# Performance work log

Measured on AMD Instinct MI355X. Metric: run time of the kernel, lower is better.

Reference implementation:

```python
import jax, jax.numpy as jnp
import numpy as np

N = 131072
L = 300  # lan_vec_len

def _boxes(k):
    k1, k2, k3, k4 = jax.random.split(k, 4)
    x1 = jax.random.uniform(k1, (N,)) * 500.0
    y1 = jax.random.uniform(k2, (N,)) * 500.0
    w = 1.0 + jax.random.uniform(k3, (N,)) * 200.0
    h = 1.0 + jax.random.uniform(k4, (N,)) * 200.0
    return x1, y1, x1 + w, y1 + h

def setup_inputs() -> dict:
    key = jax.random.key(0)
    ks = jax.random.split(key, 10)
    sbj_vec = jax.random.normal(ks[0], (N, L), jnp.float32)
    obj_vec = jax.random.normal(ks[1], (N, L), jnp.float32)
    sx1, sy1, sx2, sy2 = _boxes(ks[2])
    ox1, oy1, ox2, oy2 = _boxes(ks[3])
    label = jax.random.randint(ks[4], (N,), 0, 2).astype(jnp.float32)
    misc = jax.random.uniform(ks[5], (N,))
    # rlts columns: [0:4 misc, 4 label, 5:9 sbj box, 9 misc, 10:14 obj box, 14 misc]
    rlts = jnp.stack([misc, misc, misc, misc, label,
                      sx1, sy1, sx2, sy2, misc,
                      ox1, oy1, ox2, oy2, misc], axis=1)
    spa_w = jax.random.normal(ks[6], (8, 1), jnp.float32) * 0.1
    spa_b = jnp.zeros((1,), jnp.float32)
    lan_w1 = jax.random.normal(ks[7], (2 * L, L), jnp.float32) * 0.05
    lan_b1 = jnp.zeros((L,), jnp.float32)
    lan_w2 = jax.random.normal(ks[8], (L, 1), jnp.float32) * 0.05
    lan_b2 = jnp.zeros((1,), jnp.float32)
    return {"sbj_vec": sbj_vec, "obj_vec": obj_vec, "rlts": rlts,
            "spa_w": spa_w, "spa_b": spa_b,
            "lan_w1": lan_w1, "lan_b1": lan_b1,
            "lan_w2": lan_w2, "lan_b2": lan_b2}

def _ext_box_feat(rlts):
    sb = rlts[:, 5:9]
    ob = rlts[:, 10:14]
    sw = sb[:, 2] - sb[:, 0]
    sh = sb[:, 3] - sb[:, 1]
    ow = ob[:, 2] - ob[:, 0]
    oh = ob[:, 3] - ob[:, 1]
    sbj = jnp.stack([(sb[:, 0] - ob[:, 0]) / sw,
                     (sb[:, 1] - ob[:, 1]) / sh,
                     jnp.log(sw / ow), jnp.log(sh / oh)], axis=1)
    obj = jnp.stack([(ob[:, 0] - sb[:, 0]) / ow,
                     (ob[:, 1] - sb[:, 1]) / oh,
                     jnp.log(ow / sw), jnp.log(oh / sh)], axis=1)
    return sbj, obj

def reference(sbj_vec, obj_vec, rlts, spa_w, spa_b, lan_w1, lan_b1, lan_w2, lan_b2):
    sbj_box, obj_box = _ext_box_feat(rlts)
    lan_feat = jnp.concatenate([sbj_vec, obj_vec], axis=1)        # [N, 2L]
    box_feat = jnp.concatenate([sbj_box, obj_box], axis=1)        # [N, 8]
    # lan_stream: ReLU -> (Dropout: identity in eval) -> Linear -> ReLU -> Linear
    h = jax.nn.relu(lan_feat)
    h = jax.nn.relu(h @ lan_w1 + lan_b1)
    lan_scores = h @ lan_w2 + lan_b2                              # [N, 1]
    box_scores = box_feat @ spa_w + spa_b                         # [N, 1]
    scores = jax.nn.sigmoid(lan_scores + box_scores)              # [N, 1]
    ys = (rlts[:, 4] > 0).astype(scores.dtype)                    # [N]
    s = scores[:, 0]
    # binary cross entropy (mean), clamped like torch's BCE
    log_s = jnp.clip(jnp.log(jnp.clip(s, 1e-12, 1.0)), -100.0)
    log_1s = jnp.clip(jnp.log(jnp.clip(1.0 - s, 1e-12, 1.0)), -100.0)
    loss = -jnp.mean(ys * log_s + (1.0 - ys) * log_1s)
    # faithful replication of loss_test's (buggy) counting logic, vectorized
    neg = ys == 0
    pos = ~neg
    N_pos = jnp.sum(pos.astype(jnp.float32))
    N_neg = jnp.sum(neg.astype(jnp.float32))
    N_pos_right = jnp.sum((neg & (s >= 0.5)).astype(jnp.float32))
    N_neg_right = jnp.sum((pos & (s < 0.5)).astype(jnp.float32))
    recall_pos = N_pos_right / N_pos
    recall_neg = N_neg_right / N_neg
    recall_all = (N_pos_right + N_neg_right) / (N_pos + N_neg)
    return scores, loss, recall_pos, recall_neg, recall_all
```

## Files before the change

### kernel.cpp

```cpp
#include <hip/hip_runtime.h>

constexpr int NROWS  = 131072;
constexpr int LDIM   = 300;
constexpr int KDIM   = 600;
constexpr int NPAD   = 320;
constexpr int KGRP   = 76;
constexpr int MTILE  = 128;
constexpr int NBLKS  = NROWS / MTILE;
constexpr int KSTEPS = 19;
constexpr int WT_ELEMS = KGRP * NPAD * 8;
constexpr size_t PART_OFF = 393216;

typedef __bf16 bf16x8 __attribute__((ext_vector_type(8)));
typedef float  f32x16 __attribute__((ext_vector_type(16)));
typedef const unsigned int __attribute__((address_space(1))) gu32;
typedef unsigned int __attribute__((address_space(3))) lu32;

__device__ __forceinline__ unsigned short f2bf(float f) {
    unsigned u = __float_as_uint(f);
    u += 0x7fffu + ((u >> 16) & 1u);
    return (unsigned short)(u >> 16);
}

__global__ void prep_w1(const float* __restrict__ w1, unsigned short* __restrict__ wt) {
    int idx = blockIdx.x * 256 + threadIdx.x;
    if (idx >= WT_ELEMS) return;
    int j    = idx & 7;
    int rest = idx >> 3;
    int n    = rest % NPAD;
    int kg   = rest / NPAD;
    int k    = kg * 8 + j;
    float v = 0.f;
    if (k < KDIM && n < LDIM) v = w1[k * LDIM + n];
    wt[idx] = f2bf(v);
}

__launch_bounds__(256, 2)
__global__ void main_kernel(const float* __restrict__ sbj, const float* __restrict__ obj,
                            const float* __restrict__ rlts,
                            const float* __restrict__ spa_w, const float* __restrict__ spa_b,
                            const float* __restrict__ b1, const float* __restrict__ w2,
                            const float* __restrict__ b2,
                            const unsigned short* __restrict__ wt,
                            float* __restrict__ out_scores, float* __restrict__ part) {
    __shared__ __attribute__((aligned(16))) short A_lds[4 * 128 * 8];
    __shared__ __attribute__((aligned(16))) short B_lds[4 * 320 * 8];
    __shared__ float lanpart[2][128];
    __shared__ float redbuf[4][8];

    const int tid  = threadIdx.x;
    const int lane = tid & 63;
    const int wv   = tid >> 6;
    const int wm   = wv >> 1;
    const int wn   = wv & 1;
    const int l31  = lane & 31;
    const int l5   = lane >> 5;

    const int  blk  = blockIdx.x;
    const long row0 = (long)blk * MTILE;

    const int a_quad = tid & 7;
    const int a_rowb = tid >> 3;

    f32x16 acc[2][5];
    #pragma unroll
    for (int mt = 0; mt < 2; ++mt)
        #pragma unroll
        for (int nt = 0; nt < 5; ++nt)
            acc[mt][nt] = (f32x16)(0.f);

    for (int kt = 0; kt < KSTEPS; ++kt) {
        {
            const unsigned short* src = wt + (size_t)kt * (4 * 320 * 8) + wv * 2560 + lane * 8;
            short* dst = &B_lds[wv * 2560 + lane * 8];
            #pragma unroll
            for (int it = 0; it < 5; ++it) {
                __builtin_amdgcn_global_load_lds((gu32*)(src + it * 512),
                                                 (lu32*)(dst + it * 512), 16, 0, 0);
            }
        }
        {
            const int kglob0 = kt * 32 + a_quad * 4;
            #pragma unroll
            for (int i = 0; i < 4; ++i) {
                const int  row  = a_rowb + i * 32;
                const long grow = row0 + row;
                float4 v;
                if (kglob0 < LDIM) {
                    v = *(const float4*)(sbj + grow * LDIM + kglob0);
                } else if (kglob0 < KDIM) {
                    v = *(const float4*)(obj + grow * LDIM + (kglob0 - LDIM));
                } else {
                    v = make_float4(0.f, 0.f, 0.f, 0.f);
                }
                unsigned h0 = f2bf(fmaxf(v.x, 0.f));
                unsigned h1 = f2bf(fmaxf(v.y, 0.f));
                unsigned h2 = f2bf(fmaxf(v.z, 0.f));
                unsigned h3 = f2bf(fmaxf(v.w, 0.f));
                uint2 pk = make_uint2(h0 | (h1 << 16), h2 | (h3 << 16));
                *(uint2*)&A_lds[((a_quad >> 1) * 128 + row) * 8 + (a_quad & 1) * 4] = pk;
            }
        }
        __syncthreads();
        #pragma unroll
        for (int ki = 0; ki < 2; ++ki) {
            const int half = ki * 2 + l5;
            bf16x8 af[2];
            #pragma unroll
            for (int mt = 0; mt < 2; ++mt) {
                const int row = wm * 64 + mt * 32 + l31;
                af[mt] = *(const bf16x8*)&A_lds[(half * 128 + row) * 8];
            }
            #pragma unroll
            for (int nt = 0; nt < 5; ++nt) {
                const int n = wn * 160 + nt * 32 + l31;
                bf16x8 bfr = *(const bf16x8*)&B_lds[(half * 320 + n) * 8];
                #pragma unroll
                for (int mt = 0; mt < 2; ++mt)
                    acc[mt][nt] = __builtin_amdgcn_mfma_f32_32x32x16_bf16(af[mt], bfr, acc[mt][nt], 0, 0, 0);
            }
        }
        __syncthreads();
    }

    float part_r[2][16];
    #pragma unroll
    for (int mt = 0; mt < 2; ++mt)
        #pragma unroll
        for (int r = 0; r < 16; ++r) part_r[mt][r] = 0.f;

    #pragma unroll
    for (int nt = 0; nt < 5; ++nt) {
        const int n = wn * 160 + nt * 32 + l31;
        if (n < LDIM) {
            const float b1n = b1[n];
            const float w2n = w2[n];
            #pragma unroll
            for (int mt = 0; mt < 2; ++mt)
                #pragma unroll
                for (int r = 0; r < 16; ++r) {
                    float h = fmaxf(acc[mt][nt][r] + b1n, 0.f);
                    part_r[mt][r] = fmaf(h, w2n, part_r[mt][r]);
                }
        }
    }
    #pragma unroll
    for (int off = 1; off < 32; off <<= 1)
        #pragma unroll
        for (int mt = 0; mt < 2; ++mt)
            #pragma unroll
            for (int r = 0; r < 16; ++r)
                part_r[mt][r] += __shfl_xor(part_r[mt][r], off, 64);

    if (l31 == 0) {
        #pragma unroll
        for (int mt = 0; mt < 2; ++mt)
            #pragma unroll
            for (int r = 0; r < 16; ++r) {
                const int rl = wm * 64 + mt * 32 + (r & 3) + 8 * (r >> 2) + 4 * l5;
                lanpart[wn][rl] = part_r[mt][r];
            }
    }
    __syncthreads();

    float s_loss = 0.f, s_cp = 0.f, s_cn = 0.f, s_pr = 0.f, s_nr = 0.f;
    if (tid < 128) {
        const long g   = row0 + tid;
        const float lan = lanpart[0][tid] + lanpart[1][tid] + b2[0];
        const float* rr = rlts + g * 15;
        const float label = rr[4];
        const float sx1 = rr[5],  sy1 = rr[6],  sx2 = rr[7],  sy2 = rr[8];
        const float ox1 = rr[10], oy1 = rr[11], ox2 = rr[12], oy2 = rr[13];
        const float sw = sx2 - sx1, sh = sy2 - sy1, ow = ox2 - ox1, oh = oy2 - oy1;
        float bs = spa_w[0] * ((sx1 - ox1) / sw)
                 + spa_w[1] * ((sy1 - oy1) / sh)
                 + spa_w[2] * logf(sw / ow)
                 + spa_w[3] * logf(sh / oh)
                 + spa_w[4] * ((ox1 - sx1) / ow)
                 + spa_w[5] * ((oy1 - sy1) / oh)
                 + spa_w[6] * logf(ow / sw)
                 + spa_w[7] * logf(oh / sh)
                 + spa_b[0];
        const float z = lan + bs;
        const float s = 1.f / (1.f + expf(-z));
        out_scores[g] = s;
        const float ls = fmaxf(logf(fminf(fmaxf(s, 1e-12f), 1.f)), -100.f);
        const float l1 = fmaxf(logf(fminf(fmaxf(1.f - s, 1e-12f), 1.f)), -100.f);
        const bool ys = label > 0.f;
        s_loss = ys ? ls : l1;
        s_cp   = ys ? 1.f : 0.f;
        s_cn   = ys ? 0.f : 1.f;
        s_pr   = (!ys && s >= 0.5f) ? 1.f : 0.f;
        s_nr   = (ys && s < 0.5f)  ? 1.f : 0.f;
    }
    #pragma unroll
    for (int off = 1; off < 64; off <<= 1) {
        s_loss += __shfl_xor(s_loss, off, 64);
        s_cp   += __shfl_xor(s_cp, off, 64);
        s_cn   += __shfl_xor(s_cn, off, 64);
        s_pr   += __shfl_xor(s_pr, off, 64);
        s_nr   += __shfl_xor(s_nr, off, 64);
    }
    if (lane == 0) {
        redbuf[wv][0] = s_loss; redbuf[wv][1] = s_cp; redbuf[wv][2] = s_cn;
        redbuf[wv][3] = s_pr;   redbuf[wv][4] = s_nr;
    }
    __syncthreads();
    if (tid == 0) {
        float t0 = 0.f, t1 = 0.f, t2 = 0.f, t3 = 0.f, t4 = 0.f;
        for (int w = 0; w < 4; ++w) {
            t0 += redbuf[w][0]; t1 += redbuf[w][1]; t2 += redbuf[w][2];
            t3 += redbuf[w][3]; t4 += redbuf[w][4];
        }
        part[blk * 8 + 0] = t0; part[blk * 8 + 1] = t1; part[blk * 8 + 2] = t2;
        part[blk * 8 + 3] = t3; part[blk * 8 + 4] = t4;
    }
}

__global__ void final_reduce(const float* __restrict__ part, float* __restrict__ out) {
    __shared__ float red[4][8];
    const int tid = threadIdx.x;
    const int lane = tid & 63, wv = tid >> 6;
    float a0 = 0.f, a1 = 0.f, a2 = 0.f, a3 = 0.f, a4 = 0.f;
    for (int b = tid; b < NBLKS; b += 256) {
        a0 += part[b * 8 + 0]; a1 += part[b * 8 + 1]; a2 += part[b * 8 + 2];
        a3 += part[b * 8 + 3]; a4 += part[b * 8 + 4];
    }
    #pragma unroll
    for (int off = 1; off < 64; off <<= 1) {
        a0 += __shfl_xor(a0, off, 64); a1 += __shfl_xor(a1, off, 64);
        a2 += __shfl_xor(a2, off, 64); a3 += __shfl_xor(a3, off, 64);
        a4 += __shfl_xor(a4, off, 64);
    }
    if (lane == 0) { red[wv][0] = a0; red[wv][1] = a1; red[wv][2] = a2; red[wv][3] = a3; red[wv][4] = a4; }
    __syncthreads();
    if (tid == 0) {
        float t0 = 0.f, t1 = 0.f, t2 = 0.f, t3 = 0.f, t4 = 0.f;
        for (int w = 0; w < 4; ++w) {
            t0 += red[w][0]; t1 += red[w][1]; t2 += red[w][2]; t3 += red[w][3]; t4 += red[w][4];
        }
        out[NROWS + 0] = -t0 / (float)NROWS;
        out[NROWS + 1] = t3 / t1;
        out[NROWS + 2] = t4 / t2;
        out[NROWS + 3] = (t3 + t4) / (t1 + t2);
    }
}

extern "C" void kernel_launch(void* const* d_in, const int* in_sizes, int n_in,
                              void* d_out, int out_size, void* d_ws, size_t ws_size,
                              hipStream_t stream) {
    const float* sbj   = (const float*)d_in[0];
    const float* obj   = (const float*)d_in[1];
    const float* rlts  = (const float*)d_in[2];
    const float* spa_w = (const float*)d_in[3];
    const float* spa_b = (const float*)d_in[4];
    const float* w1    = (const float*)d_in[5];
    const float* b1    = (const float*)d_in[6];
    const float* w2    = (const float*)d_in[7];
    const float* b2    = (const float*)d_in[8];
    float* out = (float*)d_out;

    unsigned short* wt = (unsigned short*)d_ws;
    float* part = (float*)((char*)d_ws + PART_OFF);

    prep_w1<<<(WT_ELEMS + 255) / 256, 256, 0, stream>>>(w1, wt);
    main_kernel<<<NBLKS, 256, 0, stream>>>(sbj, obj, rlts, spa_w, spa_b, b1, w2, b2, wt, out, part);
    final_reduce<<<1, 256, 0, stream>>>(part, out);
}
```

Baseline: 404.7 us.

## Shrink row tile, read W1 fragments from global, double-buffer A in LDS

Halves the row tile to 64 rows per block and switches from 32x32 to 16x16x32 MFMA, with each wave covering 80 output columns across all 64 rows. The B (W1) operand is no longer staged through LDS via global_load_lds; each wave reads its bf16 fragments straight from global/L2. A is double-buffered in padded LDS, and the next k-step's global loads are issued before the MFMAs, so only one barrier is needed per step. Occupancy is raised to 3 blocks per CU. This trades more L2 traffic for W1 and twice as many blocks for less LDS use and better latency hiding.

```diff
diff --git a/kernel.cpp b/kernel.cpp
--- a/kernel.cpp
+++ b/kernel.cpp
@@ -5,16 +5,15 @@
 constexpr int KDIM   = 600;
 constexpr int NPAD   = 320;
 constexpr int KGRP   = 76;
-constexpr int MTILE  = 128;
+constexpr int MTILE  = 64;
 constexpr int NBLKS  = NROWS / MTILE;
 constexpr int KSTEPS = 19;
 constexpr int WT_ELEMS = KGRP * NPAD * 8;
 constexpr size_t PART_OFF = 393216;
+constexpr int ASTRIDE = 40;
 
 typedef __bf16 bf16x8 __attribute__((ext_vector_type(8)));
-typedef float  f32x16 __attribute__((ext_vector_type(16)));
-typedef const unsigned int __attribute__((address_space(1))) gu32;
-typedef unsigned int __attribute__((address_space(3))) lu32;
+typedef float  f32x4  __attribute__((ext_vector_type(4)));
 
 __device__ __forceinline__ unsigned short f2bf(float f) {
     unsigned u = __float_as_uint(f);
@@ -35,7 +34,7 @@
     wt[idx] = f2bf(v);
 }
 
-__launch_bounds__(256, 2)
+__launch_bounds__(256, 3)
 __global__ void main_kernel(const float* __restrict__ sbj, const float* __restrict__ obj,
                             const float* __restrict__ rlts,
                             const float* __restrict__ spa_w, const float* __restrict__ spa_b,
@@ -43,130 +42,125 @@
                             const float* __restrict__ b2,
                             const unsigned short* __restrict__ wt,
                             float* __restrict__ out_scores, float* __restrict__ part) {
-    __shared__ __attribute__((aligned(16))) short A_lds[4 * 128 * 8];
-    __shared__ __attribute__((aligned(16))) short B_lds[4 * 320 * 8];
-    __shared__ float lanpart[2][128];
+    __shared__ __attribute__((aligned(16))) short A_lds[2][MTILE * ASTRIDE];
+    __shared__ float lanpart[4][MTILE];
     __shared__ float redbuf[4][8];
 
     const int tid  = threadIdx.x;
     const int lane = tid & 63;
     const int wv   = tid >> 6;
-    const int wm   = wv >> 1;
-    const int wn   = wv & 1;
-    const int l31  = lane & 31;
-    const int l5   = lane >> 5;
+    const int l4   = lane & 15;
+    const int q4   = lane >> 4;
+    const int nbase = wv * 80;
 
     const int  blk  = blockIdx.x;
     const long row0 = (long)blk * MTILE;
 
     const int a_quad = tid & 7;
-    const int a_rowb = tid >> 3;
-
-    f32x16 acc[2][5];
-    #pragma unroll
-    for (int mt = 0; mt < 2; ++mt)
-        #pragma unroll
-        for (int nt = 0; nt < 5; ++nt)
-            acc[mt][nt] = (f32x16)(0.f);
+    const int a_row  = tid >> 3;
+
+    f32x4 acc[4][5];
+    #pragma unroll
+    for (int rt = 0; rt < 4; ++rt)
+        #pragma unroll
+        for (int ct = 0; ct < 5; ++ct)
+            acc[rt][ct] = (f32x4)(0.f);
+
+    float4 pre[2];
+
+    auto load_A = [&](int kt) {
+        const int k0 = kt * 32 + a_quad * 4;
+        #pragma unroll
+        for (int i = 0; i < 2; ++i) {
+            const long grow = row0 + a_row + i * 32;
+            if (k0 < LDIM)       pre[i] = *(const float4*)(sbj + grow * LDIM + k0);
+            else if (k0 < KDIM)  pre[i] = *(const float4*)(obj + grow * LDIM + (k0 - LDIM));
+            else                 pre[i] = make_float4(0.f, 0.f, 0.f, 0.f);
+        }
+    };
+    auto store_A = [&](int buf) {
+        #pragma unroll
+        for (int i = 0; i < 2; ++i) {
+            const int row = a_row + i * 32;
+            unsigned h0 = f2bf(fmaxf(pre[i].x, 0.f));
+            unsigned h1 = f2bf(fmaxf(pre[i].y, 0.f));
+            unsigned h2 = f2bf(fmaxf(pre[i].z, 0.f));
+            unsigned h3 = f2bf(fmaxf(pre[i].w, 0.f));
+            uint2 pk = make_uint2(h0 | (h1 << 16), h2 | (h3 << 16));
+            *(uint2*)&A_lds[buf][row * ASTRIDE + a_quad * 4] = pk;
+        }
+    };
+
+    load_A(0);
+    store_A(0);
 
     for (int kt = 0; kt < KSTEPS; ++kt) {
-        {
-            const unsigned short* src = wt + (size_t)kt * (4 * 320 * 8) + wv * 2560 + lane * 8;
-            short* dst = &B_lds[wv * 2560 + lane * 8];
-            #pragma unroll
-            for (int it = 0; it < 5; ++it) {
-                __builtin_amdgcn_global_load_lds((gu32*)(src + it * 512),
-                                                 (lu32*)(dst + it * 512), 16, 0, 0);
-            }
-        }
-        {
-            const int kglob0 = kt * 32 + a_quad * 4;
-            #pragma unroll
-            for (int i = 0; i < 4; ++i) {
-                const int  row  = a_rowb + i * 32;
-                const long grow = row0 + row;
-                float4 v;
-                if (kglob0 < LDIM) {
-                    v = *(const float4*)(sbj + grow * LDIM + kglob0);
-                } else if (kglob0 < KDIM) {
-                    v = *(const float4*)(obj + grow * LDIM + (kglob0 - LDIM));
-                } else {
-                    v = make_float4(0.f, 0.f, 0.f, 0.f);
-                }
-                unsigned h0 = f2bf(fmaxf(v.x, 0.f));
-                unsigned h1 = f2bf(fmaxf(v.y, 0.f));
-                unsigned h2 = f2bf(fmaxf(v.z, 0.f));
-                unsigned h3 = f2bf(fmaxf(v.w, 0.f));
-                uint2 pk = make_uint2(h0 | (h1 << 16), h2 | (h3 << 16));
-                *(uint2*)&A_lds[((a_quad >> 1) * 128 + row) * 8 + (a_quad & 1) * 4] = pk;
-            }
-        }
+        const int buf = kt & 1;
         __syncthreads();
-        #pragma unroll
-        for (int ki = 0; ki < 2; ++ki) {
-            const int half = ki * 2 + l5;
-            bf16x8 af[2];
-            #pragma unroll
-            for (int mt = 0; mt < 2; ++mt) {
-                const int row = wm * 64 + mt * 32 + l31;
-                af[mt] = *(const bf16x8*)&A_lds[(half * 128 + row) * 8];
-            }
-            #pragma unroll
-            for (int nt = 0; nt < 5; ++nt) {
-                const int n = wn * 160 + nt * 32 + l31;
-                bf16x8 bfr = *(const bf16x8*)&B_lds[(half * 320 + n) * 8];
-                #pragma unroll
-                for (int mt = 0; mt < 2; ++mt)
-                    acc[mt][nt] = __builtin_amdgcn_mfma_f32_32x32x16_bf16(af[mt], bfr, acc[mt][nt], 0, 0, 0);
-            }
-        }
-        __syncthreads();
-    }
-
-    float part_r[2][16];
-    #pragma unroll
-    for (int mt = 0; mt < 2; ++mt)
-        #pragma unroll
-        for (int r = 0; r < 16; ++r) part_r[mt][r] = 0.f;
-
-    #pragma unroll
-    for (int nt = 0; nt < 5; ++nt) {
-        const int n = wn * 160 + nt * 32 + l31;
+        if (kt + 1 < KSTEPS) load_A(kt + 1);
+
+        bf16x8 af[4];
+        #pragma unroll
+        for (int rt = 0; rt < 4; ++rt)
+            af[rt] = *(const bf16x8*)&A_lds[buf][(rt * 16 + l4) * ASTRIDE + q4 * 8];
+
+        bf16x8 bfr[5];
+        #pragma unroll
+        for (int ct = 0; ct < 5; ++ct) {
+            const int kg = kt * 4 + q4;
+            bfr[ct] = *(const bf16x8*)(wt + ((size_t)kg * NPAD + nbase + ct * 16 + l4) * 8);
+        }
+        #pragma unroll
+        for (int ct = 0; ct < 5; ++ct)
+            #pragma unroll
+            for (int rt = 0; rt < 4; ++rt)
+                acc[rt][ct] = __builtin_amdgcn_mfma_f32_16x16x32_bf16(af[rt], bfr[ct], acc[rt][ct], 0, 0, 0);
+
+        if (kt + 1 < KSTEPS) store_A(buf ^ 1);
+    }
+
+    float part_r[4][4];
+    #pragma unroll
+    for (int rt = 0; rt < 4; ++rt)
+        #pragma unroll
+        for (int r = 0; r < 4; ++r) part_r[rt][r] = 0.f;
+
+    #pragma unroll
+    for (int ct = 0; ct < 5; ++ct) {
+        const int n = nbase + ct * 16 + l4;
         if (n < LDIM) {
             const float b1n = b1[n];
             const float w2n = w2[n];
             #pragma unroll
-            for (int mt = 0; mt < 2; ++mt)
+            for (int rt = 0; rt < 4; ++rt)
                 #pragma unroll
-                for (int r = 0; r < 16; ++r) {
-                    float h = fmaxf(acc[mt][nt][r] + b1n, 0.f);
-                    part_r[mt][r] = fmaf(h, w2n, part_r[mt][r]);
+                for (int r = 0; r < 4; ++r) {
+                    float h = fmaxf(acc[rt][ct][r] + b1n, 0.f);
+                    part_r[rt][r] = fmaf(h, w2n, part_r[rt][r]);
                 }
         }
     }
     #pragma unroll
-    for (int off = 1; off < 32; off <<= 1)
-        #pragma unroll
-        for (int mt = 0; mt < 2; ++mt)
-            #pragma unroll
-            for (int r = 0; r < 16; ++r)
-                part_r[mt][r] += __shfl_xor(part_r[mt][r], off, 64);
-
-    if (l31 == 0) {
-        #pragma unroll
-        for (int mt = 0; mt < 2; ++mt)
-            #pragma unroll
-            for (int r = 0; r < 16; ++r) {
-                const int rl = wm * 64 + mt * 32 + (r & 3) + 8 * (r >> 2) + 4 * l5;
-                lanpart[wn][rl] = part_r[mt][r];
-            }
+    for (int off = 1; off < 16; off <<= 1)
+        #pragma unroll
+        for (int rt = 0; rt < 4; ++rt)
+            #pragma unroll
+            for (int r = 0; r < 4; ++r)
+                part_r[rt][r] += __shfl_xor(part_r[rt][r], off, 64);
+
+    if (l4 == 0) {
+        #pragma unroll
+        for (int rt = 0; rt < 4; ++rt)
+            #pragma unroll
+            for (int r = 0; r < 4; ++r)
+                lanpart[wv][rt * 16 + q4 * 4 + r] = part_r[rt][r];
     }
     __syncthreads();
 
     float s_loss = 0.f, s_cp = 0.f, s_cn = 0.f, s_pr = 0.f, s_nr = 0.f;
-    if (tid < 128) {
+    if (tid < MTILE) {
         const long g   = row0 + tid;
-        const float lan = lanpart[0][tid] + lanpart[1][tid] + b2[0];
+        const float lan = lanpart[0][tid] + lanpart[1][tid] + lanpart[2][tid] + lanpart[3][tid] + b2[0];
         const float* rr = rlts + g * 15;
         const float label = rr[4];
         const float sx1 = rr[5],  sy1 = rr[6],  sx2 = rr[7],  sy2 = rr[8];
```

Result: faster. 384.0 us (-5.1%).
